# Kernel optimization log

Measured on AMD Instinct MI355X. Metric: run time of the kernel, lower is better.

Reference implementation:

```python
import jax, jax.numpy as jnp
import numpy as np

N_NODES = 50000
N_EDGES = 800000
IN_CH = 128
OUT_CH = 64
HEADS = 1
NEG_SLOPE = 0.2

def _glorot(key, shape):
    stdv = np.sqrt(6.0 / (shape[-2] + shape[-1]))
    return jax.random.uniform(key, shape, jnp.float32, -stdv, stdv)

def setup_inputs() -> dict:
    key = jax.random.key(0)
    k1, k2, k3, k4, k5 = jax.random.split(key, 5)
    x = jax.random.normal(k1, (N_NODES, IN_CH), jnp.float32)
    src = jax.random.randint(k2, (N_EDGES,), 0, N_NODES)
    dst = jax.random.randint(k3, (N_EDGES,), 0, N_NODES)
    # ensure no pre-existing self loops (remove_self_loops is then identity)
    dst = jnp.where(src == dst, (dst + 1) % N_NODES, dst)
    edge_index = jnp.stack([src, dst]).astype(jnp.int64)
    weight = _glorot(k4, (IN_CH, HEADS * OUT_CH))
    att = _glorot(k5, (1, HEADS, 2 * OUT_CH))
    bias = jnp.zeros((OUT_CH,), jnp.float32)
    return {"x": x, "edge_index": edge_index, "weight": weight, "att": att, "bias": bias}

def reference(x, edge_index, weight, att, bias):
    N = x.shape[0]
    # linear projection -> [N, heads, out]
    h = (x @ weight).reshape(N, HEADS, OUT_CH)
    # add self loops (input guaranteed free of self loops)
    loops = jnp.arange(N, dtype=edge_index.dtype)
    src = jnp.concatenate([edge_index[0], loops])  # source j
    dst = jnp.concatenate([edge_index[1], loops])  # target i
    x_j = h[src]   # [E+N, heads, out]
    x_i = h[dst]
    # attention logits: (cat([x_i, x_j]) * att).sum(-1) -> [E+N, heads]
    alpha = jnp.concatenate([x_i, x_j], axis=-1)
    alpha = (alpha * att).sum(axis=-1)
    alpha = jax.nn.leaky_relu(alpha, NEG_SLOPE)
    # segment softmax over destination nodes
    amax = jax.ops.segment_max(alpha, dst, num_segments=N)
    e = jnp.exp(alpha - amax[dst])
    esum = jax.ops.segment_sum(e, dst, num_segments=N)
    alpha = e / (esum[dst] + 1e-16)
    # message + scatter-add aggregation
    msg = x_j * alpha[:, :, None]
    out = jax.ops.segment_sum(msg, dst, num_segments=N)  # [N, heads, out]
    out = out.mean(axis=1) + bias
    # F.normalize (L2, dim=1, eps=1e-12); dropout is eval-mode identity
    norm = jnp.maximum(jnp.linalg.norm(out, axis=1, keepdims=True), 1e-12)
    return out / norm
```

## Files before the change

kernel.cpp:

```cpp
#include <hip/hip_runtime.h>
#include <math.h>

#define IN_CH 128
#define OUT_CH 64
#define NEG_SLOPE 0.2f
#define CAP 32

__device__ __forceinline__ unsigned short f2bf(float f) {
    unsigned u = __float_as_uint(f);
    unsigned r = (u + 0x7FFFu + ((u >> 16) & 1u)) >> 16;
    return (unsigned short)r;
}

__device__ __forceinline__ bool sniff_is64(const void* edges) {
    const unsigned* up = (const unsigned*)edges;
    bool is64 = true;
#pragma unroll
    for (int k = 0; k < 16; k++) is64 = is64 && (up[2 * k + 1] == 0u);
    return is64;
}

__global__ __launch_bounds__(256) void k_mm_cs(
        const float* __restrict__ x, const float* __restrict__ W,
        const float* __restrict__ att, unsigned short* __restrict__ h16,
        float* __restrict__ asrc, float* __restrict__ adst, int N,
        const void* __restrict__ edges, int* __restrict__ counts,
        unsigned short* __restrict__ slots, int* __restrict__ oflow_cnt,
        int2* __restrict__ oflow, int E, int mmb, int csb) {
    __shared__ float Ws[64 * OUT_CH];
    int t = threadIdx.x;
    int bid = blockIdx.x;
    int lo = min(mmb, csb), M2 = 2 * lo;
    int role, id;
    if (bid < M2) { role = bid & 1; id = bid >> 1; }
    else          { role = (mmb > csb) ? 0 : 1; id = bid - M2 + lo; }

    if (role == 1) {
        int e0 = (id * 256 + t) * 2;
        if (e0 >= E) return;
        bool has1 = (e0 + 1 < E);
        int s0, s1 = 0, d0, d1 = 0;
        if (sniff_is64(edges)) {
            const long long* p = (const long long*)edges;
            int4 vs = *(const int4*)&p[e0];
            int4 vd = *(const int4*)&p[(size_t)E + e0];
            s0 = vs.x; s1 = vs.z;
            d0 = vd.x; d1 = vd.z;
        } else {
            const int* p = (const int*)edges;
            int2 vs = *(const int2*)&p[e0];
            int2 vd = *(const int2*)&p[E + e0];
            s0 = vs.x; s1 = vs.y;
            d0 = vd.x; d1 = vd.y;
        }
        int r0 = atomicAdd(counts + d0, 1);
        if (r0 < CAP) slots[((size_t)d0 << 5) + r0] = (unsigned short)s0;
        else {
            int p2 = atomicAdd(oflow_cnt, 1);
            oflow[p2] = make_int2(s0, d0);
        }
        if (has1) {
            int r1 = atomicAdd(counts + d1, 1);
            if (r1 < CAP) slots[((size_t)d1 << 5) + r1] = (unsigned short)s1;
            else {
                int p2 = atomicAdd(oflow_cnt, 1);
                oflow[p2] = make_int2(s1, d1);
            }
        }
        return;
    }

    int cg = t & 15, g = t >> 4;
    float4 att_d = *(const float4*)&att[cg * 4];
    float4 att_s = *(const float4*)&att[64 + cg * 4];

    int n0 = id * 64 + g * 4;
    int nn[4];
#pragma unroll
    for (int m = 0; m < 4; m++) nn[m] = min(n0 + m, N - 1);

    float4 acc[4];
#pragma unroll
    for (int m = 0; m < 4; m++) acc[m] = make_float4(0.f, 0.f, 0.f, 0.f);

    const int HALF = 64 * OUT_CH;
#pragma unroll
    for (int h = 0; h < 2; h++) {
        if (h) __syncthreads();
        for (int i = t * 4; i < HALF; i += 256 * 4)
            *(float4*)&Ws[i] = *(const float4*)&W[h * HALF + i];
        __syncthreads();
#pragma unroll 2
        for (int k4 = 0; k4 < 16; k4++) {
            float4 xv[4];
#pragma unroll
            for (int m = 0; m < 4; m++)
                xv[m] = *(const float4*)&x[(size_t)nn[m] * IN_CH + h * 64 + k4 * 4];
            float4 wv[4];
#pragma unroll
            for (int j = 0; j < 4; j++)
                wv[j] = *(const float4*)&Ws[(k4 * 4 + j) * OUT_CH + cg * 4];
#pragma unroll
            for (int m = 0; m < 4; m++) {
                acc[m].x = fmaf(xv[m].x, wv[0].x, acc[m].x);
                acc[m].y = fmaf(xv[m].x, wv[0].y, acc[m].y);
                acc[m].z = fmaf(xv[m].x, wv[0].z, acc[m].z);
                acc[m].w = fmaf(xv[m].x, wv[0].w, acc[m].w);
                acc[m].x = fmaf(xv[m].y, wv[1].x, acc[m].x);
                acc[m].y = fmaf(xv[m].y, wv[1].y, acc[m].y);
                acc[m].z = fmaf(xv[m].y, wv[1].z, acc[m].z);
                acc[m].w = fmaf(xv[m].y, wv[1].w, acc[m].w);
                acc[m].x = fmaf(xv[m].z, wv[2].x, acc[m].x);
                acc[m].y = fmaf(xv[m].z, wv[2].y, acc[m].y);
                acc[m].z = fmaf(xv[m].z, wv[2].z, acc[m].z);
                acc[m].w = fmaf(xv[m].z, wv[2].w, acc[m].w);
                acc[m].x = fmaf(xv[m].w, wv[3].x, acc[m].x);
                acc[m].y = fmaf(xv[m].w, wv[3].y, acc[m].y);
                acc[m].z = fmaf(xv[m].w, wv[3].z, acc[m].z);
                acc[m].w = fmaf(xv[m].w, wv[3].w, acc[m].w);
            }
        }
    }

#pragma unroll
    for (int m = 0; m < 4; m++) {
        int node = n0 + m;
        if (node < N) {
            ushort4 hv;
            hv.x = f2bf(acc[m].x);
            hv.y = f2bf(acc[m].y);
            hv.z = f2bf(acc[m].z);
            hv.w = f2bf(acc[m].w);
            *(ushort4*)&h16[(size_t)node * OUT_CH + cg * 4] = hv;
        }
        float pd = acc[m].x * att_d.x + acc[m].y * att_d.y +
                   acc[m].z * att_d.z + acc[m].w * att_d.w;
        float ps = acc[m].x * att_s.x + acc[m].y * att_s.y +
                   acc[m].z * att_s.z + acc[m].w * att_s.w;
#pragma unroll
        for (int msk = 1; msk < 16; msk <<= 1) {
            pd += __shfl_xor(pd, msk, 64);
            ps += __shfl_xor(ps, msk, 64);
        }
        if (cg == 0 && node < N) { adst[node] = pd; asrc[node] = ps; }
    }
}

__global__ __launch_bounds__(256) void k_agg(const unsigned short* __restrict__ h16,
                                             const unsigned short* __restrict__ slots,
                                             const int* __restrict__ counts,
                                             const int* __restrict__ oflow_cnt,
                                             const int2* __restrict__ oflow,
                                             const float* __restrict__ asrc,
                                             const float* __restrict__ adst,
                                             const float* __restrict__ bias,
                                             float* __restrict__ out, int N) {
    __shared__ float2 stage[4][64];
    int lane = threadIdx.x & 63;
    int wid = threadIdx.x >> 6;
    int node = blockIdx.x * 4 + wid;
    if (node >= N) return;
    int half = lane >> 5;
    int ch2 = (lane & 31) * 2;

    float aD = adst[node];
    float a = aD + asrc[node];
    a = a > 0.f ? a : NEG_SLOPE * a;
    float w_self = __expf(a);
    unsigned hv = *(const unsigned*)&h16[(size_t)node * OUT_CH + ch2];
    float wse = half ? 0.f : w_self;
    float accx = wse * __uint_as_float(hv << 16);
    float accy = wse * __uint_as_float(hv & 0xFFFF0000u);

    int c = counts[node];
    int cs = min(c, CAP);
    int sv = 0;
    float wv = 0.f;
    if (lane < cs) {
        sv = (int)slots[((size_t)node << 5) + lane];
        float av = aD + asrc[sv];
        av = av > 0.f ? av : NEG_SLOPE * av;
        wv = __expf(av);
    }
    float esum_lane = wv;
    stage[wid][lane] = make_float2(__int_as_float(sv), wv);

    for (int j = 0; j < cs; j += 16) {
#pragma unroll
        for (int k = 0; k < 8; k++) {
            float2 p = stage[wid][j + 2 * k + half];
            int s = __float_as_int(p.x);
            unsigned v = *(const unsigned*)&h16[((size_t)s << 6) + ch2];
            accx = fmaf(p.y, __uint_as_float(v << 16), accx);
            accy = fmaf(p.y, __uint_as_float(v & 0xFFFF0000u), accy);
        }
    }
    accx += __shfl_xor(accx, 32, 64);
    accy += __shfl_xor(accy, 32, 64);
#pragma unroll
    for (int m = 32; m >= 1; m >>= 1) esum_lane += __shfl_xor(esum_lane, m, 64);
    float esum = esum_lane + w_self;

    int oc = *oflow_cnt;
    if (oc > 0) {
        for (int i = 0; i < oc; i++) {
            int2 e = oflow[i];
            if (e.y == node) {
                float av = aD + asrc[e.x];
                av = av > 0.f ? av : NEG_SLOPE * av;
                float w = __expf(av);
                esum += w;
                unsigned v = *(const unsigned*)&h16[((size_t)e.x << 6) + ch2];
                accx = fmaf(w, __uint_as_float(v << 16), accx);
                accy = fmaf(w, __uint_as_float(v & 0xFFFF0000u), accy);
            }
        }
    }

    float inv = 1.f / (esum + 1e-16f);
    float2 bv = *(const float2*)&bias[ch2];
    float vx = accx * inv + bv.x;
    float vy = accy * inv + bv.y;
    float ss = vx * vx + vy * vy;
#pragma unroll
    for (int m = 16; m >= 1; m >>= 1) ss += __shfl_xor(ss, m, 64);
    float rinv = 1.f / fmaxf(sqrtf(ss), 1e-12f);
    if (!half)
        *(float2*)&out[(size_t)node * OUT_CH + ch2] = make_float2(vx * rinv, vy * rinv);
}

extern "C" void kernel_launch(void* const* d_in, const int* in_sizes, int n_in,
                              void* d_out, int out_size, void* d_ws, size_t ws_size,
                              hipStream_t stream) {
    const float* x    = (const float*)d_in[0];
    const void*  edges = d_in[1];
    const float* W    = (const float*)d_in[2];
    const float* att  = (const float*)d_in[3];
    const float* bias = (const float*)d_in[4];
    float* out = (float*)d_out;

    const int N = in_sizes[0] / IN_CH;
    const int E = in_sizes[1] / 2;
    const int MMB = (N + 63) / 64;
    const int CSB = ((E + 1) / 2 + 255) / 256;

    char* ws = (char*)d_ws;
    size_t off = 0;
    auto alloc = [&](size_t bytes) -> void* {
        void* p = ws + off;
        off += bytes;
        off = (off + 255) & ~(size_t)255;
        return p;
    };
    int*            counts    = (int*)alloc((size_t)(N + 64) * 4);
    unsigned short* slots     = (unsigned short*)alloc((size_t)N * CAP * 2);
    int2*           oflow     = (int2*)alloc((size_t)E * 8);
    unsigned short* h16       = (unsigned short*)alloc((size_t)N * OUT_CH * 2);
    float*          asrc      = (float*)alloc((size_t)N * 4);
    float*          adst      = (float*)alloc((size_t)N * 4);
    int*            oflow_cnt = counts + N;

    hipMemsetAsync(counts, 0, (size_t)(N + 64) * 4, stream);
    k_mm_cs<<<MMB + CSB, 256, 0, stream>>>(x, W, att, h16, asrc, adst, N,
                                           edges, counts, slots, oflow_cnt,
                                           oflow, E, MMB, CSB);
    k_agg<<<(N + 3) / 4, 256, 0, stream>>>(h16, slots, counts, oflow_cnt, oflow,
                                           asrc, adst, bias, out, N);
}
```

Baseline: 145.6 us.

## Partition edge scatter into destination buckets and interleave node ordering in aggregation

The counting-sort scatter now runs as 8 bucket passes per edge chunk. Each block re-reads a 2048-edge chunk and handles only the destinations with dst mod 8 equal to its bucket, presumably to localize atomics and slot writes per bucket or XCD. The aggregation kernel remaps node indices so each block slot handles nodes with a fixed mod-8 residue, matching that partitioning. In exchange, destination indices are read eight times over and the block scheduling becomes more complex.

```diff
diff --git a/kernel.cpp b/kernel.cpp
--- a/kernel.cpp
+++ b/kernel.cpp
@@ -20,61 +20,121 @@
     return is64;
 }
 
-__global__ __launch_bounds__(256) void k_mm_cs(
+__global__ __launch_bounds__(256) void k_fused(
         const float* __restrict__ x, const float* __restrict__ W,
         const float* __restrict__ att, unsigned short* __restrict__ h16,
         float* __restrict__ asrc, float* __restrict__ adst, int N,
         const void* __restrict__ edges, int* __restrict__ counts,
         unsigned short* __restrict__ slots, int* __restrict__ oflow_cnt,
-        int2* __restrict__ oflow, int E, int mmb, int csb) {
+        int2* __restrict__ oflow, int E, int mmb) {
     __shared__ float Ws[64 * OUT_CH];
     int t = threadIdx.x;
     int bid = blockIdx.x;
-    int lo = min(mmb, csb), M2 = 2 * lo;
-    int role, id;
-    if (bid < M2) { role = bid & 1; id = bid >> 1; }
-    else          { role = (mmb > csb) ? 0 : 1; id = bid - M2 + lo; }
-
-    if (role == 1) {
-        int e0 = (id * 256 + t) * 2;
-        if (e0 >= E) return;
-        bool has1 = (e0 + 1 < E);
-        int s0, s1 = 0, d0, d1 = 0;
-        if (sniff_is64(edges)) {
+    int g = bid >> 4;
+    int k = bid & 15;
+
+    if (k < 8) {
+        int bucket = k;
+        long base = (long)g * 2048;
+        if (base >= E) return;
+        bool is64 = sniff_is64(edges);
+        if (is64 && !(E & 1)) {
             const long long* p = (const long long*)edges;
-            int4 vs = *(const int4*)&p[e0];
-            int4 vd = *(const int4*)&p[(size_t)E + e0];
-            s0 = vs.x; s1 = vs.z;
-            d0 = vd.x; d1 = vd.z;
+#pragma unroll
+            for (int it = 0; it < 4; it++) {
+                long e = base + (it * 256 + t) * 2;
+                if (e + 1 < E) {
+                    int4 vd = *(const int4*)&p[E + e];
+                    if ((vd.x & 7) == bucket) {
+                        int s = (int)p[e];
+                        int r = atomicAdd(counts + vd.x, 1);
+                        if (r < CAP) slots[((size_t)vd.x << 5) + r] = (unsigned short)s;
+                        else { int q = atomicAdd(oflow_cnt, 1); oflow[q] = make_int2(s, vd.x); }
+                    }
+                    if ((vd.z & 7) == bucket) {
+                        int s = (int)p[e + 1];
+                        int r = atomicAdd(counts + vd.z, 1);
+                        if (r < CAP) slots[((size_t)vd.z << 5) + r] = (unsigned short)s;
+                        else { int q = atomicAdd(oflow_cnt, 1); oflow[q] = make_int2(s, vd.z); }
+                    }
+                } else if (e < E) {
+                    int d = (int)p[E + e];
+                    if ((d & 7) == bucket) {
+                        int s = (int)p[e];
+                        int r = atomicAdd(counts + d, 1);
+                        if (r < CAP) slots[((size_t)d << 5) + r] = (unsigned short)s;
+                        else { int q = atomicAdd(oflow_cnt, 1); oflow[q] = make_int2(s, d); }
+                    }
+                }
+            }
+        } else if (is64) {
+            const long long* p = (const long long*)edges;
+            for (int it = 0; it < 8; it++) {
+                long e = base + it * 256 + t;
+                if (e >= E) break;
+                int d = (int)p[E + e];
+                if ((d & 7) == bucket) {
+                    int s = (int)p[e];
+                    int r = atomicAdd(counts + d, 1);
+                    if (r < CAP) slots[((size_t)d << 5) + r] = (unsigned short)s;
+                    else { int q = atomicAdd(oflow_cnt, 1); oflow[q] = make_int2(s, d); }
+                }
+            }
         } else {
             const int* p = (const int*)edges;
-            int2 vs = *(const int2*)&p[e0];
-            int2 vd = *(const int2*)&p[E + e0];
-            s0 = vs.x; s1 = vs.y;
-            d0 = vd.x; d1 = vd.y;
-        }
-        int r0 = atomicAdd(counts + d0, 1);
-        if (r0 < CAP) slots[((size_t)d0 << 5) + r0] = (unsigned short)s0;
-        else {
-            int p2 = atomicAdd(oflow_cnt, 1);
-            oflow[p2] = make_int2(s0, d0);
-        }
-        if (has1) {
-            int r1 = atomicAdd(counts + d1, 1);
-            if (r1 < CAP) slots[((size_t)d1 << 5) + r1] = (unsigned short)s1;
-            else {
-                int p2 = atomicAdd(oflow_cnt, 1);
-                oflow[p2] = make_int2(s1, d1);
+            bool a4 = ((E & 3) == 0);
+            if (a4) {
+#pragma unroll
+                for (int it = 0; it < 2; it++) {
+                    long e = base + (it * 256 + t) * 4;
+                    if (e + 3 < E) {
+                        int4 vd = *(const int4*)&p[E + e];
+                        int dd[4] = {vd.x, vd.y, vd.z, vd.w};
+#pragma unroll
+                        for (int i = 0; i < 4; i++) {
+                            if ((dd[i] & 7) == bucket) {
+                                int s = p[e + i];
+                                int r = atomicAdd(counts + dd[i], 1);
+                                if (r < CAP) slots[((size_t)dd[i] << 5) + r] = (unsigned short)s;
+                                else { int q = atomicAdd(oflow_cnt, 1); oflow[q] = make_int2(s, dd[i]); }
+                            }
+                        }
+                    } else {
+                        for (long e2 = e; e2 < E && e2 < e + 4; e2++) {
+                            int d = p[E + e2];
+                            if ((d & 7) == bucket) {
+                                int s = p[e2];
+                                int r = atomicAdd(counts + d, 1);
+                                if (r < CAP) slots[((size_t)d << 5) + r] = (unsigned short)s;
+                                else { int q = atomicAdd(oflow_cnt, 1); oflow[q] = make_int2(s, d); }
+                            }
+                        }
+                    }
+                }
+            } else {
+                for (int it = 0; it < 8; it++) {
+                    long e = base + it * 256 + t;
+                    if (e >= E) break;
+                    int d = p[E + e];
+                    if ((d & 7) == bucket) {
+                        int s = p[e];
+                        int r = atomicAdd(counts + d, 1);
+                        if (r < CAP) slots[((size_t)d << 5) + r] = (unsigned short)s;
+                        else { int q = atomicAdd(oflow_cnt, 1); oflow[q] = make_int2(s, d); }
+                    }
+                }
             }
         }
         return;
     }
 
-    int cg = t & 15, g = t >> 4;
+    int id = g * 8 + (k - 8);
+    if (id >= mmb) return;
+    int cg = t & 15, gg = t >> 4;
     float4 att_d = *(const float4*)&att[cg * 4];
     float4 att_s = *(const float4*)&att[64 + cg * 4];
 
-    int n0 = id * 64 + g * 4;
+    int n0 = id * 64 + gg * 4;
     int nn[4];
 #pragma unroll
     for (int m = 0; m < 4; m++) nn[m] = min(n0 + m, N - 1);
@@ -158,7 +218,9 @@
     __shared__ float2 stage[4][64];
     int lane = threadIdx.x & 63;
     int wid = threadIdx.x >> 6;
-    int node = blockIdx.x * 4 + wid;
+    int b = blockIdx.x & 7;
+    int kk = blockIdx.x >> 3;
+    int node = b + 8 * (kk * 4 + wid);
     if (node >= N) return;
     int half = lane >> 5;
     int ch2 = (lane & 31) * 2;
@@ -242,7 +304,10 @@
     const int N = in_sizes[0] / IN_CH;
     const int E = in_sizes[1] / 2;
     const int MMB = (N + 63) / 64;
-    const int CSB = ((E + 1) / 2 + 255) / 256;
+    const int CH  = (E + 2047) / 2048;
+    const int GM  = (MMB + 7) / 8;
+    const int G   = (CH > GM ? CH : GM);
+    const int GRID = G * 16;
 
     char* ws = (char*)d_ws;
     size_t off = 0;
@@ -261,9 +326,11 @@
     int*            oflow_cnt = counts + N;
 
     hipMemsetAsync(counts, 0, (size_t)(N + 64) * 4, stream);
-    k_mm_cs<<<MMB + CSB, 256, 0, stream>>>(x, W, att, h16, asrc, adst, N,
-                                           edges, counts, slots, oflow_cnt,
-                                           oflow, E, MMB, CSB);
-    k_agg<<<(N + 3) / 4, 256, 0, stream>>>(h16, slots, counts, oflow_cnt, oflow,
-                                           asrc, adst, bias, out, N);
-}
+    k_fused<<<GRID, 256, 0, stream>>>(x, W, att, h16, asrc, adst, N,
+                                      edges, counts, slots, oflow_cnt,
+                                      oflow, E, MMB);
+    const int NP  = (N + 7) / 8;
+    const int AGB = 8 * ((NP + 3) / 4);
+    k_agg<<<AGB, 256, 0, stream>>>(h16, slots, counts, oflow_cnt, oflow,
+                                   asrc, adst, bias, out, N);
+}
```

Result: slower. 154.7 us (+6.2%).
